# Kernel tuning notes

Hardware: AMD Instinct MI355X
Metric: run time of the kernel (lower is better)

The kernel has to match this reference:

```python
import jax, jax.numpy as jnp
import numpy as np

N_NODES = 50000
N_EDGES = 800000
HIDDEN = 128
NUM_BASIS = 32
CUTOFF = 5.0


def setup_inputs() -> dict:
    key = jax.random.key(0)
    ks = jax.random.split(key, 9)
    node_features = jax.random.normal(ks[0], (N_NODES, HIDDEN), dtype=jnp.float32)
    positions = jax.random.normal(ks[1], (N_NODES, 3), dtype=jnp.float32)
    edge_index = jax.random.randint(ks[2], (2, N_EDGES), 0, N_NODES)
    edge_in = 2 * HIDDEN + NUM_BASIS
    W1 = jax.random.normal(ks[3], (edge_in, HIDDEN), dtype=jnp.float32) * (edge_in ** -0.5)
    b1 = jnp.zeros((HIDDEN,), dtype=jnp.float32)
    W2 = jax.random.normal(ks[4], (HIDDEN, HIDDEN), dtype=jnp.float32) * (HIDDEN ** -0.5)
    b2 = jnp.zeros((HIDDEN,), dtype=jnp.float32)
    Wo = jax.random.normal(ks[5], (HIDDEN, HIDDEN), dtype=jnp.float32) * (HIDDEN ** -0.5)
    bo = jnp.zeros((HIDDEN,), dtype=jnp.float32)
    return dict(node_features=node_features, positions=positions, edge_index=edge_index,
                W1=W1, b1=b1, W2=W2, b2=b2, Wo=Wo, bo=bo)


def reference(node_features, positions, edge_index, W1, b1, W2, b2, Wo, bo):
    n_nodes = node_features.shape[0]
    # Gaussian radial basis (fixed buffers)
    centers = jnp.linspace(0.0, CUTOFF, NUM_BASIS)  # [NB]
    width = 0.5 * (centers[1] - centers[0] + 0.01)
    src, dst = edge_index[0], edge_index[1]
    rel = positions[dst] - positions[src]                       # [E,3]
    dist = jnp.linalg.norm(rel, axis=-1)                        # [E]
    d = jnp.minimum(dist, CUTOFF)
    rbf = jnp.exp(-0.5 * ((d[:, None] - centers) / width) ** 2)  # [E,NB]
    # edge message: concat(src feats, dst feats, rbf) -> 2-layer SiLU MLP
    msg = jnp.concatenate([node_features[src], node_features[dst], rbf], axis=-1)  # [E,2H+NB]
    h = jax.nn.silu(msg @ W1 + b1) @ W2 + b2                    # [E,H]
    # scatter-add to destination nodes + degree normalization
    updates = jax.ops.segment_sum(h, dst, num_segments=n_nodes)          # [N,H]
    degree = jax.ops.segment_sum(jnp.ones_like(dist), dst, num_segments=n_nodes)
    updates = updates / jnp.maximum(degree, 1.0)[:, None]
    return updates @ Wo + bo
```

## Files before the change

### kernel.cpp

```cpp
#include <hip/hip_runtime.h>

#define NN 50000
#define NE 800000
#define HID 128
#define NB 32
#define SCAN_B 196

typedef short short8 __attribute__((ext_vector_type(8)));
typedef float f32x4 __attribute__((ext_vector_type(4)));

static __device__ __forceinline__ short f2bf(float x) {
    unsigned int u = __float_as_uint(x);
    unsigned int r = (u + 0x7fffu + ((u >> 16) & 1u)) >> 16;
    return (short)r;
}

static __device__ __forceinline__ unsigned int addpack(unsigned int a, unsigned int b) {
    float lo = __uint_as_float(a << 16) + __uint_as_float(b << 16);
    float hi = __uint_as_float(a & 0xffff0000u) + __uint_as_float(b & 0xffff0000u);
    return ((unsigned int)(unsigned short)f2bf(hi) << 16) | (unsigned short)f2bf(lo);
}

__global__ void fused_prep(const int* __restrict__ dstI, int* __restrict__ counts,
                           const float* __restrict__ W1, const float* __restrict__ W2,
                           const float* __restrict__ Wo,
                           short* __restrict__ W1aT, short* __restrict__ W1bT,
                           short* __restrict__ W1cT, short* __restrict__ W2t,
                           short* __restrict__ Wot) {
    int b = blockIdx.x;
    if (b < 3125) {
        int e = b * 256 + threadIdx.x;
        atomicAdd(&counts[dstI[e]], 1);
    } else {
        int t = (b - 3125) * 256 + threadIdx.x;
        if (t < 16384) {
            int n = t >> 7, k = t & 127;
            W1aT[t] = f2bf(W1[k * HID + n]);
        } else if ((t -= 16384) < 16384) {
            int n = t >> 7, k = t & 127;
            W1bT[t] = f2bf(W1[(k + 128) * HID + n]);
        } else if ((t -= 16384) < 4096) {
            int n = t >> 5, k = t & 31;
            W1cT[t] = f2bf(W1[(k + 256) * HID + n]);
        } else if ((t -= 4096) < 16384) {
            int n = t >> 7, k = t & 127;
            W2t[t] = f2bf(W2[k * HID + n]);
        } else if ((t -= 16384) < 16384) {
            int n = t >> 7, k = t & 127;
            Wot[t] = f2bf(Wo[k * HID + n]);
        }
    }
}

__global__ void k_scan1(const int* __restrict__ counts, int* __restrict__ scanEx,
                        int* __restrict__ blockSum) {
    __shared__ int s[256];
    int t = threadIdx.x, idx = blockIdx.x * 256 + t;
    int v = counts[idx];
    s[t] = v; __syncthreads();
    #pragma unroll
    for (int off = 1; off < 256; off <<= 1) {
        int x = (t >= off) ? s[t - off] : 0;
        __syncthreads();
        s[t] += x;
        __syncthreads();
    }
    scanEx[idx] = s[t] - v;
    if (t == 255) blockSum[blockIdx.x] = s[255];
}

__global__ void k_scan2(const int* __restrict__ blockSum, int* __restrict__ blockBase) {
    __shared__ int s[256];
    int t = threadIdx.x;
    int v = (t < SCAN_B) ? blockSum[t] : 0;
    s[t] = v; __syncthreads();
    #pragma unroll
    for (int off = 1; off < 256; off <<= 1) {
        int x = (t >= off) ? s[t - off] : 0;
        __syncthreads();
        s[t] += x;
        __syncthreads();
    }
    blockBase[t] = s[t] - v;
}

__global__ void k_scan3(const int* __restrict__ scanEx, const int* __restrict__ blockBase,
                        int* __restrict__ cur) {
    int idx = blockIdx.x * 256 + threadIdx.x;
    cur[idx] = scanEx[idx] + blockBase[blockIdx.x];
}

__global__ void k_permute(const int* __restrict__ src, const int* __restrict__ dst,
                          int* __restrict__ cur, int2* __restrict__ edgeS) {
    int e = blockIdx.x * 256 + threadIdx.x;
    int s = src[e];
    int d = dst[e];
    int r = atomicAdd(&cur[d], 1);
    edgeS[r] = make_int2(s, d);
}

__global__ void sd_kernel(const float* __restrict__ nf,
                          const short* __restrict__ W1aT, const short* __restrict__ W1bT,
                          short* __restrict__ Sg, short* __restrict__ Dg) {
    __shared__ short As[64 * 136];
    const int tid  = threadIdx.x;
    const int wave = tid >> 6;
    const int lane = tid & 63;
    const int quad = lane >> 4;
    const int l15  = lane & 15;
    const int n0   = blockIdx.x * 64;

    {
        int row = tid >> 2, pt = tid & 3;
        int node = min(n0 + row, NN - 1);
        const float4* p = (const float4*)(nf + (size_t)node * HID + pt * 32);
        #pragma unroll
        for (int j = 0; j < 4; ++j) {
            float4 w0 = p[j * 2], w1 = p[j * 2 + 1];
            short8 o;
            o[0] = f2bf(w0.x); o[1] = f2bf(w0.y); o[2] = f2bf(w0.z); o[3] = f2bf(w0.w);
            o[4] = f2bf(w1.x); o[5] = f2bf(w1.y); o[6] = f2bf(w1.z); o[7] = f2bf(w1.w);
            *(short8*)(As + row * 136 + pt * 32 + j * 8) = o;
        }
    }
    __syncthreads();

    f32x4 aS[4][2], aD[4][2];
    #pragma unroll
    for (int mt = 0; mt < 4; ++mt)
        #pragma unroll
        for (int nt = 0; nt < 2; ++nt) {
            aS[mt][nt] = (f32x4){0.f, 0.f, 0.f, 0.f};
            aD[mt][nt] = (f32x4){0.f, 0.f, 0.f, 0.f};
        }

    #pragma unroll
    for (int kk = 0; kk < 4; ++kk) {
        int ko = kk * 32 + quad * 8;
        short8 a[4];
        #pragma unroll
        for (int mt = 0; mt < 4; ++mt)
            a[mt] = *(const short8*)(As + (mt * 16 + l15) * 136 + ko);
        #pragma unroll
        for (int nt = 0; nt < 2; ++nt) {
            int n = wave * 32 + nt * 16 + l15;
            short8 bS = *(const short8*)(W1aT + n * HID + ko);
            short8 bD = *(const short8*)(W1bT + n * HID + ko);
            #pragma unroll
            for (int mt = 0; mt < 4; ++mt) {
                aS[mt][nt] = __builtin_amdgcn_mfma_f32_16x16x32_bf16(a[mt], bS, aS[mt][nt], 0, 0, 0);
                aD[mt][nt] = __builtin_amdgcn_mfma_f32_16x16x32_bf16(a[mt], bD, aD[mt][nt], 0, 0, 0);
            }
        }
    }

    #pragma unroll
    for (int nt = 0; nt < 2; ++nt) {
        int col = wave * 32 + nt * 16 + l15;
        #pragma unroll
        for (int mt = 0; mt < 4; ++mt) {
            #pragma unroll
            for (int r = 0; r < 4; ++r) {
                int node = n0 + mt * 16 + quad * 4 + r;
                if (node < NN) {
                    Sg[(size_t)node * HID + col] = f2bf(aS[mt][nt][r]);
                    Dg[(size_t)node * HID + col] = f2bf(aD[mt][nt][r]);
                }
            }
        }
    }
}

__launch_bounds__(512, 6)
__global__ void edge_kernel(const short* __restrict__ Sg,
                            const short* __restrict__ Dg,
                            const float* __restrict__ pos,
                            const int2* __restrict__ edgeS,
                            const short* __restrict__ W1cT,
                            const float* __restrict__ b1,
                            const short* __restrict__ W2t,
                            const float* __restrict__ b2,
                            float* __restrict__ upd) {
    __shared__ char buf[49152];
    __shared__ int  dn_sh[128];
    short* PRE = (short*)buf;
    short* R   = (short*)(buf + 34816);
    short* Ps  = (short*)buf;
    float* UfT = (float*)buf;

    const int tid  = threadIdx.x;
    const int wave = tid >> 6;
    const int lane = tid & 63;
    const int quad = lane >> 4;
    const int l15  = lane & 15;
    const int mg   = wave >> 2;
    const int nsl  = wave & 3;
    const int e0   = blockIdx.x * 128;

    {
        int es = tid >> 2, pt = tid & 3;
        int2 sd = edgeS[e0 + es];
        int s = sd.x, d = sd.y;
        const int4* sp = (const int4*)(Sg + (size_t)s * HID + pt * 32);
        const int4* dp = (const int4*)(Dg + (size_t)d * HID + pt * 32);
        int4* op = (int4*)(PRE + es * 136 + pt * 32);
        #pragma unroll
        for (int j = 0; j < 4; ++j) {
            int4 a = sp[j], b = dp[j];
            int4 o;
            o.x = addpack(a.x, b.x);
            o.y = addpack(a.y, b.y);
            o.z = addpack(a.z, b.z);
            o.w = addpack(a.w, b.w);
            op[j] = o;
        }
        if (pt == 0) dn_sh[es] = d;
        float dx = pos[d * 3 + 0] - pos[s * 3 + 0];
        float dy = pos[d * 3 + 1] - pos[s * 3 + 1];
        float dz = pos[d * 3 + 2] - pos[s * 3 + 2];
        float dd = fminf(sqrtf(dx * dx + dy * dy + dz * dz), 5.0f);
        const float step  = 5.0f / 31.0f;
        const float width = 0.5f * (step + 0.01f);
        const float coef  = -0.5f / (width * width);
        short8 r;
        #pragma unroll
        for (int j = 0; j < 8; ++j) {
            float c = step * (float)(pt * 8 + j);
            float t = dd - c;
            r[j] = f2bf(__expf(coef * t * t));
        }
        *(short8*)(R + es * 56 + pt * 8) = r;
    }
    __syncthreads();

    f32x4 acc[4][2];
    #pragma unroll
    for (int mt = 0; mt < 4; ++mt)
        #pragma unroll
        for (int nt = 0; nt < 2; ++nt) acc[mt][nt] = (f32x4){0.f, 0.f, 0.f, 0.f};
    {
        int ko = quad * 8;
        short8 a[4];
        #pragma unroll
        for (int mt = 0; mt < 4; ++mt)
            a[mt] = *(const short8*)(R + (mg * 64 + mt * 16 + l15) * 56 + ko);
        #pragma unroll
        for (int nt = 0; nt < 2; ++nt) {
            int n = nsl * 32 + nt * 16 + l15;
            short8 b = *(const short8*)(W1cT + n * NB + ko);
            #pragma unroll
            for (int mt = 0; mt < 4; ++mt)
                acc[mt][nt] = __builtin_amdgcn_mfma_f32_16x16x32_bf16(a[mt], b, acc[mt][nt], 0, 0, 0);
        }
    }

    {
        float b1c[2] = { b1[nsl * 32 + l15], b1[nsl * 32 + 16 + l15] };
        const unsigned short* PREu = (const unsigned short*)PRE;
        #pragma unroll
        for (int nt = 0; nt < 2; ++nt) {
            int col = nsl * 32 + nt * 16 + l15;
            #pragma unroll
            for (int mt = 0; mt < 4; ++mt) {
                #pragma unroll
                for (int r = 0; r < 4; ++r) {
                    int row = mg * 64 + mt * 16 + quad * 4 + r;
                    float pre = __uint_as_float((unsigned int)PREu[row * 136 + col] << 16);
                    float x = acc[mt][nt][r] + pre + b1c[nt];
                    float p = x / (1.0f + __expf(-x));
                    Ps[row * 136 + col] = f2bf(p);
                }
            }
        }
    }
    __syncthreads();

    f32x4 acc2[4][2];
    #pragma unroll
    for (int mt = 0; mt < 4; ++mt)
        #pragma unroll
        for (int nt = 0; nt < 2; ++nt) acc2[mt][nt] = (f32x4){0.f, 0.f, 0.f, 0.f};

    #pragma unroll
    for (int kk = 0; kk < 4; ++kk) {
        int ko = kk * 32 + quad * 8;
        short8 a[4];
        #pragma unroll
        for (int mt = 0; mt < 4; ++mt)
            a[mt] = *(const short8*)(Ps + (mg * 64 + mt * 16 + l15) * 136 + ko);
        #pragma unroll
        for (int nt = 0; nt < 2; ++nt) {
            int n = nsl * 32 + nt * 16 + l15;
            short8 b = *(const short8*)(W2t + n * HID + ko);
            #pragma unroll
            for (int mt = 0; mt < 4; ++mt)
                acc2[mt][nt] = __builtin_amdgcn_mfma_f32_16x16x32_bf16(a[mt], b, acc2[mt][nt], 0, 0, 0);
        }
    }
    __syncthreads();

    float b2c[2] = { b2[nsl * 32 + l15], b2[nsl * 32 + 16 + l15] };
    #pragma unroll
    for (int h = 0; h < 2; ++h) {
        if (mg == h) {
            #pragma unroll
            for (int nt = 0; nt < 2; ++nt) {
                int col = nsl * 32 + nt * 16 + l15;
                #pragma unroll
                for (int mt = 0; mt < 4; ++mt) {
                    f32x4 v;
                    #pragma unroll
                    for (int r = 0; r < 4; ++r) v[r] = acc2[mt][nt][r] + b2c[nt];
                    *(f32x4*)(UfT + col * 68 + mt * 16 + quad * 4) = v;
                }
            }
        }
        __syncthreads();
        {
            int col = tid & 127;
            int seg = tid >> 7;
            int rb  = h * 64 + seg * 16;
            const float* cp = UfT + col * 68 + seg * 16;
            f32x4 vv[4];
            #pragma unroll
            for (int j = 0; j < 4; ++j) vv[j] = *(const f32x4*)(cp + j * 4);
            int rnode = dn_sh[rb];
            float run = 0.0f;
            #pragma unroll
            for (int i = 0; i < 16; ++i) {
                int node = dn_sh[rb + i];
                float v = vv[i >> 2][i & 3];
                if (node != rnode) {
                    atomicAdd(upd + (size_t)rnode * HID + col, run);
                    rnode = node;
                    run = v;
                } else {
                    run += v;
                }
            }
            atomicAdd(upd + (size_t)rnode * HID + col, run);
        }
        __syncthreads();
    }
}

__launch_bounds__(256, 4)
__global__ void out_kernel(float* __restrict__ out,
                           const int* __restrict__ counts,
                           const short* __restrict__ Wot,
                           const float* __restrict__ bo) {
    __shared__ short A2[64 * 136];

    const int tid  = threadIdx.x;
    const int wave = tid >> 6;
    const int lane = tid & 63;
    const int quad = lane >> 4;
    const int l15  = lane & 15;
    const int n0   = blockIdx.x * 64;

    {
        int row = tid >> 2, pt = tid & 3;
        int node = n0 + row;
        if (node < NN) {
            float inv = 1.0f / fmaxf((float)counts[node], 1.0f);
            const float4* p = (const float4*)(out + (size_t)node * HID + pt * 32);
            #pragma unroll
            for (int j = 0; j < 4; ++j) {
                float4 w0 = p[j * 2], w1 = p[j * 2 + 1];
                short8 o;
                o[0] = f2bf(w0.x * inv); o[1] = f2bf(w0.y * inv);
                o[2] = f2bf(w0.z * inv); o[3] = f2bf(w0.w * inv);
                o[4] = f2bf(w1.x * inv); o[5] = f2bf(w1.y * inv);
                o[6] = f2bf(w1.z * inv); o[7] = f2bf(w1.w * inv);
                *(short8*)(A2 + row * 136 + pt * 32 + j * 8) = o;
            }
        } else {
            short8 z = (short8){0, 0, 0, 0, 0, 0, 0, 0};
            #pragma unroll
            for (int j = 0; j < 4; ++j)
                *(short8*)(A2 + row * 136 + pt * 32 + j * 8) = z;
        }
    }
    __syncthreads();

    f32x4 acc[4][2];
    #pragma unroll
    for (int mt = 0; mt < 4; ++mt)
        #pragma unroll
        for (int nt = 0; nt < 2; ++nt) acc[mt][nt] = (f32x4){0.f, 0.f, 0.f, 0.f};

    #pragma unroll
    for (int kk = 0; kk < 4; ++kk) {
        int ko = kk * 32 + quad * 8;
        short8 a[4];
        #pragma unroll
        for (int mt = 0; mt < 4; ++mt)
            a[mt] = *(const short8*)(A2 + (mt * 16 + l15) * 136 + ko);
        #pragma unroll
        for (int nt = 0; nt < 2; ++nt) {
            int n = wave * 32 + nt * 16 + l15;
            short8 b = *(const short8*)(Wot + n * HID + ko);
            #pragma unroll
            for (int mt = 0; mt < 4; ++mt)
                acc[mt][nt] = __builtin_amdgcn_mfma_f32_16x16x32_bf16(a[mt], b, acc[mt][nt], 0, 0, 0);
        }
    }
    __syncthreads();

    #pragma unroll
    for (int nt = 0; nt < 2; ++nt) {
        int col = wave * 32 + nt * 16 + l15;
        float bias = bo[col];
        #pragma unroll
        for (int mt = 0; mt < 4; ++mt) {
            #pragma unroll
            for (int r = 0; r < 4; ++r) {
                int row = mt * 16 + quad * 4 + r;
                int node = n0 + row;
                if (node < NN)
                    out[(size_t)node * HID + col] = acc[mt][nt][r] + bias;
            }
        }
    }
}

extern "C" void kernel_launch(void* const* d_in, const int* in_sizes, int n_in,
                              void* d_out, int out_size, void* d_ws, size_t ws_size,
                              hipStream_t stream) {
    const float* nf  = (const float*)d_in[0];
    const float* pos = (const float*)d_in[1];
    const int*   ei  = (const int*)d_in[2];
    const float* W1  = (const float*)d_in[3];
    const float* b1  = (const float*)d_in[4];
    const float* W2  = (const float*)d_in[5];
    const float* b2  = (const float*)d_in[6];
    const float* Wo  = (const float*)d_in[7];
    const float* bo  = (const float*)d_in[8];
    float* out = (float*)d_out;

    char* ws = (char*)d_ws;
    short* W1aT     = (short*)(ws);
    short* W1bT     = (short*)(ws + 32768);
    short* W1cT     = (short*)(ws + 65536);
    short* W2t      = (short*)(ws + 73728);
    short* Wot      = (short*)(ws + 106496);
    int*   counts   = (int*)(ws + 139264);
    int*   scanEx   = (int*)(ws + 339968);
    int*   blockSum = (int*)(ws + 540672);
    int*   blockBase= (int*)(ws + 541696);
    int*   cur      = (int*)(ws + 542720);
    int2*  edgeS    = (int2*)(ws + 743424);
    short* Sg       = (short*)(ws + 7143424);
    short* Dg       = (short*)(ws + 19943424);

    hipMemsetAsync(out, 0, (size_t)NN * HID * sizeof(float), stream);
    hipMemsetAsync(counts, 0, 200704, stream);

    fused_prep<<<3397, 256, 0, stream>>>(ei + NE, counts, W1, W2, Wo,
                                         W1aT, W1bT, W1cT, W2t, Wot);
    k_scan1<<<SCAN_B, 256, 0, stream>>>(counts, scanEx, blockSum);
    k_scan2<<<1, 256, 0, stream>>>(blockSum, blockBase);
    k_scan3<<<SCAN_B, 256, 0, stream>>>(scanEx, blockBase, cur);
    k_permute<<<3125, 256, 0, stream>>>(ei, ei + NE, cur, edgeS);
    sd_kernel<<<(NN + 63) / 64, 256, 0, stream>>>(nf, W1aT, W1bT, Sg, Dg);
    edge_kernel<<<NE / 128, 512, 0, stream>>>(Sg, Dg, pos, edgeS,
                                              W1cT, b1, W2t, b2, out);
    out_kernel<<<(NN + 63) / 64, 256, 0, stream>>>(out, counts, Wot, bo);
}
```

Measured before the change: 345.8 us.

## Merge scan stages, permute edge indices, and use bf16 intrinsics

```diff
diff --git a/kernel.cpp b/kernel.cpp
--- a/kernel.cpp
+++ b/kernel.cpp
@@ -1,4 +1,5 @@
 #include <hip/hip_runtime.h>
+#include <hip/hip_bf16.h>
 
 #define NN 50000
 #define NE 800000
@@ -10,15 +11,18 @@
 typedef float f32x4 __attribute__((ext_vector_type(4)));
 
 static __device__ __forceinline__ short f2bf(float x) {
-    unsigned int u = __float_as_uint(x);
-    unsigned int r = (u + 0x7fffu + ((u >> 16) & 1u)) >> 16;
-    return (short)r;
-}
-
+    union { __hip_bfloat16 h; short s; } r;
+    r.h = __float2bfloat16(x);
+    return r.s;
+}
+static __device__ __forceinline__ float bf2f(unsigned short s) {
+    return __uint_as_float(((unsigned int)s) << 16);
+}
 static __device__ __forceinline__ unsigned int addpack(unsigned int a, unsigned int b) {
-    float lo = __uint_as_float(a << 16) + __uint_as_float(b << 16);
-    float hi = __uint_as_float(a & 0xffff0000u) + __uint_as_float(b & 0xffff0000u);
-    return ((unsigned int)(unsigned short)f2bf(hi) << 16) | (unsigned short)f2bf(lo);
+    union { unsigned int u; __hip_bfloat162 h; } x, y, r;
+    x.u = a; y.u = b;
+    r.h = __hadd2(x.h, y.h);
+    return r.u;
 }
 
 __global__ void fused_prep(const int* __restrict__ dstI, int* __restrict__ counts,
@@ -69,34 +73,27 @@
     if (t == 255) blockSum[blockIdx.x] = s[255];
 }
 
-__global__ void k_scan2(const int* __restrict__ blockSum, int* __restrict__ blockBase) {
+__global__ void k_scan23(const int* __restrict__ scanEx, const int* __restrict__ blockSum,
+                         int* __restrict__ cur) {
     __shared__ int s[256];
-    int t = threadIdx.x;
-    int v = (t < SCAN_B) ? blockSum[t] : 0;
-    s[t] = v; __syncthreads();
-    #pragma unroll
-    for (int off = 1; off < 256; off <<= 1) {
-        int x = (t >= off) ? s[t - off] : 0;
+    int t = threadIdx.x, b = blockIdx.x;
+    s[t] = (t < b) ? blockSum[t] : 0;
+    __syncthreads();
+    #pragma unroll
+    for (int off = 128; off > 0; off >>= 1) {
+        if (t < off) s[t] += s[t + off];
         __syncthreads();
-        s[t] += x;
-        __syncthreads();
-    }
-    blockBase[t] = s[t] - v;
-}
-
-__global__ void k_scan3(const int* __restrict__ scanEx, const int* __restrict__ blockBase,
-                        int* __restrict__ cur) {
-    int idx = blockIdx.x * 256 + threadIdx.x;
-    cur[idx] = scanEx[idx] + blockBase[blockIdx.x];
-}
-
-__global__ void k_permute(const int* __restrict__ src, const int* __restrict__ dst,
-                          int* __restrict__ cur, int2* __restrict__ edgeS) {
+    }
+    int idx = b * 256 + t;
+    cur[idx] = scanEx[idx] + s[0];
+}
+
+__global__ void k_permute(const int* __restrict__ dst,
+                          int* __restrict__ cur, int* __restrict__ perm) {
     int e = blockIdx.x * 256 + threadIdx.x;
-    int s = src[e];
     int d = dst[e];
     int r = atomicAdd(&cur[d], 1);
-    edgeS[r] = make_int2(s, d);
+    perm[r] = e;
 }
 
 __global__ void sd_kernel(const float* __restrict__ nf,
@@ -175,7 +172,9 @@
 __global__ void edge_kernel(const short* __restrict__ Sg,
                             const short* __restrict__ Dg,
                             const float* __restrict__ pos,
-                            const int2* __restrict__ edgeS,
+                            const int* __restrict__ perm,
+                            const int* __restrict__ srcI,
+                            const int* __restrict__ dstI,
                             const short* __restrict__ W1cT,
                             const float* __restrict__ b1,
                             const short* __restrict__ W2t,
@@ -199,8 +198,8 @@
 
     {
         int es = tid >> 2, pt = tid & 3;
-        int2 sd = edgeS[e0 + es];
-        int s = sd.x, d = sd.y;
+        int pe = perm[e0 + es];
+        int s = srcI[pe], d = dstI[pe];
         const int4* sp = (const int4*)(Sg + (size_t)s * HID + pt * 32);
         const int4* dp = (const int4*)(Dg + (size_t)d * HID + pt * 32);
         int4* op = (int4*)(PRE + es * 136 + pt * 32);
@@ -265,9 +264,9 @@
                 #pragma unroll
                 for (int r = 0; r < 4; ++r) {
                     int row = mg * 64 + mt * 16 + quad * 4 + r;
-                    float pre = __uint_as_float((unsigned int)PREu[row * 136 + col] << 16);
+                    float pre = bf2f(PREu[row * 136 + col]);
                     float x = acc[mt][nt][r] + pre + b1c[nt];
-                    float p = x / (1.0f + __expf(-x));
+                    float p = x * __builtin_amdgcn_rcpf(1.0f + __expf(-x));
                     Ps[row * 136 + col] = f2bf(p);
                 }
             }
@@ -445,25 +444,23 @@
     short* W2t      = (short*)(ws + 73728);
     short* Wot      = (short*)(ws + 106496);
     int*   counts   = (int*)(ws + 139264);
-    int*   scanEx   = (int*)(ws + 339968);
+    int*   cur      = (int*)(ws + 339968);
     int*   blockSum = (int*)(ws + 540672);
-    int*   blockBase= (int*)(ws + 541696);
-    int*   cur      = (int*)(ws + 542720);
-    int2*  edgeS    = (int2*)(ws + 743424);
-    short* Sg       = (short*)(ws + 7143424);
-    short* Dg       = (short*)(ws + 19943424);
-
-    hipMemsetAsync(out, 0, (size_t)NN * HID * sizeof(float), stream);
-    hipMemsetAsync(counts, 0, 200704, stream);
+    int*   perm     = (int*)(ws + 541696);
+    short* Sg       = (short*)(ws + 3741696);
+    short* Dg       = (short*)(ws + 16541696);
+    int*   scanEx   = (int*)Sg;
+
+    (void)hipMemsetAsync(out, 0, (size_t)NN * HID * sizeof(float), stream);
+    (void)hipMemsetAsync(counts, 0, 200704, stream);
 
     fused_prep<<<3397, 256, 0, stream>>>(ei + NE, counts, W1, W2, Wo,
                                          W1aT, W1bT, W1cT, W2t, Wot);
     k_scan1<<<SCAN_B, 256, 0, stream>>>(counts, scanEx, blockSum);
-    k_scan2<<<1, 256, 0, stream>>>(blockSum, blockBase);
-    k_scan3<<<SCAN_B, 256, 0, stream>>>(scanEx, blockBase, cur);
-    k_permute<<<3125, 256, 0, stream>>>(ei, ei + NE, cur, edgeS);
+    k_scan23<<<SCAN_B, 256, 0, stream>>>(scanEx, blockSum, cur);
+    k_permute<<<3125, 256, 0, stream>>>(ei + NE, cur, perm);
     sd_kernel<<<(NN + 63) / 64, 256, 0, stream>>>(nf, W1aT, W1bT, Sg, Dg);
-    edge_kernel<<<NE / 128, 512, 0, stream>>>(Sg, Dg, pos, edgeS,
+    edge_kernel<<<NE / 128, 512, 0, stream>>>(Sg, Dg, pos, perm, ei, ei + NE,
                                               W1cT, b1, W2t, b2, out);
     out_kernel<<<(NN + 63) / 64, 256, 0, stream>>>(out, counts, Wot, bo);
 }
```

Result: faster. 332.3 us (-3.9%).
